# Optimization experiments

Hardware: AMD Instinct MI355X
Metric: run time of the kernel (lower is better)

## Reference

```python
import jax, jax.numpy as jnp
import numpy as np

N_NODES = 50000
N_EDGES = 800000
F_IN = 128   # in_feats
H = 256      # h_feats
C = 32       # num_classes
E_IN = 2     # raw edge feature dim
EPS = 1e-12  # F.normalize eps


def _lin_params(key, fan_in, fan_out):
    kw, kb = jax.random.split(key)
    bound = 1.0 / np.sqrt(fan_in)
    W = jax.random.uniform(kw, (fan_in, fan_out), jnp.float32, -bound, bound)
    b = jax.random.uniform(kb, (fan_out,), jnp.float32, -bound, bound)
    return W, b


def setup_inputs() -> dict:
    key = jax.random.key(0)
    ks = jax.random.split(key, 12)
    inp = {
        "node_feat": jax.random.normal(ks[0], (N_NODES, F_IN), jnp.float32),
        "edge_feat": jax.random.normal(ks[1], (N_EDGES, E_IN), jnp.float32),
        "src": jax.random.randint(ks[2], (N_EDGES,), 0, N_NODES, jnp.int32),
        "dst": jax.random.randint(ks[3], (N_EDGES,), 0, N_NODES, jnp.int32),
    }
    # conv1: SAGEConv(F_IN, H, 2, F_IN)
    inp["We1"], inp["be1"] = _lin_params(ks[4], E_IN, F_IN)        # e_linear
    inp["Wr1a"], inp["br1a"] = _lin_params(ks[5], F_IN, F_IN)      # reduce_linear1
    inp["Wr1b"], inp["br1b"] = _lin_params(ks[6], F_IN, F_IN)      # reduce_linear2
    inp["Wl1"], inp["bl1"] = _lin_params(ks[7], 2 * F_IN, H)       # linear1
    # conv2: SAGEConv(H, C, F_IN, H)
    inp["We2"], inp["be2"] = _lin_params(ks[8], F_IN, H)
    inp["Wr2a"], inp["br2a"] = _lin_params(ks[9], H, H)
    inp["Wr2b"], inp["br2b"] = _lin_params(ks[10], H, H)
    inp["Wl2"], inp["bl2"] = _lin_params(ks[11], 2 * H, C)
    return inp


def _sage_conv(h, e, src, dst, We, be, Wra, bra, Wrb, brb, Wl, bl):
    # edge weight transform
    w = e @ We + be                                    # [E, e_out]
    hs = h[src]                                        # [E, F] gather
    hd = h[dst]
    # per-edge cosine similarity (scalar per edge)
    sn = hs / jnp.maximum(jnp.linalg.norm(hs, axis=1, keepdims=True), EPS)
    dn = hd / jnp.maximum(jnp.linalg.norm(hd, axis=1, keepdims=True), EPS)
    cos = jnp.sum(sn * dn, axis=1, keepdims=True)      # [E, 1]
    m = cos * w * hs                                   # message [E, F]
    # mailbox MLP applied per-edge, then mean-reduce per dst node
    r = jax.nn.relu(m @ Wra + bra)
    r = jax.nn.relu(r @ Wrb + brb)
    s = jax.ops.segment_sum(r, dst, num_segments=N_NODES)
    cnt = jax.ops.segment_sum(jnp.ones((dst.shape[0], 1), r.dtype), dst,
                              num_segments=N_NODES)
    h_N = s / jnp.maximum(cnt, 1.0)                    # zero-degree nodes -> 0
    h_out = jnp.concatenate([h, h_N], axis=1) @ Wl + bl
    return h_out, w


def reference(node_feat, edge_feat, src, dst,
              We1, be1, Wr1a, br1a, Wr1b, br1b, Wl1, bl1,
              We2, be2, Wr2a, br2a, Wr2b, br2b, Wl2, bl2):
    h, e_h = _sage_conv(node_feat, edge_feat, src, dst,
                        We1, be1, Wr1a, br1a, Wr1b, br1b, Wl1, bl1)
    h, e_h = jax.nn.relu(h), jax.nn.relu(e_h)
    h, _ = _sage_conv(h, e_h, src, dst,
                      We2, be2, Wr2a, br2a, Wr2b, br2b, Wl2, bl2)
    return h  # [N_NODES, C] logits
```

## Files before the change

kernel.cpp:

```cpp
#include <hip/hip_runtime.h>
#include <math.h>

#define NN 50000
#define NE 800000

typedef short bf8 __attribute__((ext_vector_type(8)));
typedef short bf4v __attribute__((ext_vector_type(4)));
typedef short bf2v __attribute__((ext_vector_type(2)));
typedef float f4 __attribute__((ext_vector_type(4)));

__device__ __forceinline__ short f2b(float f) {
  unsigned int u = __float_as_uint(f);
  unsigned int r = (u + 0x7FFFu + ((u >> 16) & 1u)) >> 16;
  return (short)(unsigned short)r;
}
__device__ __forceinline__ float b2f(short s) {
  return __uint_as_float(((unsigned int)(unsigned short)s) << 16);
}
__device__ __forceinline__ f4 b2f4(bf4v p) {
  f4 v;
  v[0] = b2f(p[0]); v[1] = b2f(p[1]); v[2] = b2f(p[2]); v[3] = b2f(p[3]);
  return v;
}


__global__ __launch_bounds__(256) void prep_k(
    const float* __restrict__ Wr1a, const float* __restrict__ Wr1b,
    const float* __restrict__ We2,  const float* __restrict__ Wr2a,
    const float* __restrict__ Wr2b, const float* __restrict__ Wl1,
    short* __restrict__ WaT1, short* __restrict__ WbT1,
    short* __restrict__ We2T, short* __restrict__ WaT2,
    short* __restrict__ WbT2, short* __restrict__ Wl1T,
    const float* __restrict__ nf, short* __restrict__ nfb,
    const int* __restrict__ dst, int* __restrict__ cnt)
{
  const int b = blockIdx.x;
  if (b < 1024) {
    const float* in; short* out; int K, N, bb;
    if (b < 64)       { in = Wr1a; out = WaT1; K = 128; N = 128; bb = b; }
    else if (b < 128) { in = Wr1b; out = WbT1; K = 128; N = 128; bb = b - 64; }
    else if (b < 256) { in = We2;  out = We2T; K = 128; N = 256; bb = b - 128; }
    else if (b < 512) { in = Wr2a; out = WaT2; K = 256; N = 256; bb = b - 256; }
    else if (b < 768) { in = Wr2b; out = WbT2; K = 256; N = 256; bb = b - 512; }
    else              { in = Wl1;  out = Wl1T; K = 256; N = 256; bb = b - 768; }
    const int i = bb * 256 + threadIdx.x;
    if (i < K * N) {
      const int n = i / K, k = i - n * K;
      out[i] = f2b(in[(size_t)k * N + n]);
    }
  } else if (b < 7274) {
    const int i = (b - 1024) * 256 + threadIdx.x;
    f4 v = *(const f4*)&nf[(size_t)i * 4];
    bf4v p;
    p[0] = f2b(v[0]); p[1] = f2b(v[1]); p[2] = f2b(v[2]); p[3] = f2b(v[3]);
    *(bf4v*)&nfb[(size_t)i * 4] = p;
  } else {
    const int e = (b - 7274) * 256 + threadIdx.x;
    atomicAdd(&cnt[dst[e]], 1);
  }
}

__global__ __launch_bounds__(256) void norm1_k(const short* __restrict__ nfb,
                                               float* __restrict__ invn) {
  const int node = blockIdx.x * 4 + (threadIdx.x >> 6);
  if (node >= NN) return;
  const int lane = threadIdx.x & 63;
  bf2v hb = *(const bf2v*)&nfb[(size_t)node * 128 + lane * 2];
  float h0 = b2f(hb[0]), h1v = b2f(hb[1]);
  float ss = fmaf(h0, h0, h1v * h1v);
#pragma unroll
  for (int o = 32; o >= 1; o >>= 1) ss += __shfl_xor(ss, o);
  if (lane == 0) invn[node] = 1.f / fmaxf(sqrtf(ss), 1e-12f);
}

__global__ __launch_bounds__(256) void norm2_k(const short* __restrict__ h1b,
                                               float* __restrict__ invn) {
  const int node = blockIdx.x * 4 + (threadIdx.x >> 6);
  if (node >= NN) return;
  const int lane = threadIdx.x & 63;
  f4 h = b2f4(*(const bf4v*)&h1b[(size_t)node * 256 + lane * 4]);
  float ss = 0.f;
#pragma unroll
  for (int r = 0; r < 4; ++r) ss = fmaf(h[r], h[r], ss);
#pragma unroll
  for (int o = 32; o >= 1; o >>= 1) ss += __shfl_xor(ss, o);
  if (lane == 0) invn[node] = 1.f / fmaxf(sqrtf(ss), 1e-12f);
}


__global__ __launch_bounds__(1024) void scanA_k(const int* __restrict__ cnt,
                                                int* __restrict__ off2,
                                                int* __restrict__ bsum) {
  __shared__ int buf[1024];
  const int t = threadIdx.x;
  const int i = blockIdx.x * 1024 + t;
  const int v = (i < NN) ? cnt[i] : 0;
  buf[t] = v;
  __syncthreads();
#pragma unroll
  for (int o = 1; o < 1024; o <<= 1) {
    int x = (t >= o) ? buf[t - o] : 0;
    __syncthreads();
    buf[t] += x;
    __syncthreads();
  }
  if (i < NN) off2[i] = buf[t] - v;
  if (t == 1023) bsum[blockIdx.x] = buf[t];
}

__global__ __launch_bounds__(64) void scanB_k(int* __restrict__ bsum, int nb) {
  const int t = threadIdx.x;
  int v = (t < nb) ? bsum[t] : 0;
#pragma unroll
  for (int o = 1; o < 64; o <<= 1) {
    int x = __shfl_up(v, o);
    if (t >= o) v += x;
  }
  if (t < nb) bsum[t] = v;
}

__global__ __launch_bounds__(256) void scanC_k(int* __restrict__ off2,
                                               const int* __restrict__ bsum) {
  const int i = blockIdx.x * 256 + threadIdx.x;
  if (i >= NN) return;
  const int b = i >> 10;
  if (b) off2[i] += bsum[b - 1];
}

__global__ __launch_bounds__(256) void perm_k(const int* __restrict__ dst,
                                              int* __restrict__ off2,
                                              int* __restrict__ perm,
                                              int* __restrict__ dsts) {
  int e = blockIdx.x * 256 + threadIdx.x;
  if (e >= NE) return;
  int d = dst[e];
  int p = atomicAdd(&off2[d], 1);
  perm[p] = e;
  dsts[p] = d;
}


__global__ __launch_bounds__(512, 8) void edge_mlp1(
    const short* __restrict__ nfb, const float* __restrict__ ef,
    const int* __restrict__ src, const int* __restrict__ perm,
    const int* __restrict__ dsts, const float* __restrict__ invn1,
    const float* __restrict__ We1, const float* __restrict__ be1,
    const short* __restrict__ WaT, const float* __restrict__ ba,
    const short* __restrict__ WbT, const float* __restrict__ bbv,
    float* __restrict__ s1)
{
  __shared__ __align__(16) short Ms[64 * 136];
  __shared__ int dse[64];
  __shared__ int sse[64];
  __shared__ float2 efs[64];
  const int t = threadIdx.x;
  const int e0 = blockIdx.x * 64;
  const int lane = t & 63, wv = t >> 6;

  if (t < 64) {
    const int pe = perm[e0 + t];
    dse[t] = dsts[e0 + t];
    sse[t] = src[pe];
    efs[t] = *(const float2*)&ef[2 * pe];
  }
  __syncthreads();

  {
    const int k2 = lane * 2;
    const float wA0 = We1[k2],       wA1 = We1[k2 + 1];
    const float wB0 = We1[128 + k2], wB1 = We1[128 + k2 + 1];
    const float bE0 = be1[k2],       bE1 = be1[k2 + 1];
    bf2v hbv[8], dbv[8];
#pragma unroll
    for (int i = 0; i < 8; ++i) {
      const int e = wv * 8 + i;
      hbv[i] = *(const bf2v*)&nfb[(size_t)sse[e] * 128 + k2];
      dbv[i] = *(const bf2v*)&nfb[(size_t)dse[e] * 128 + k2];
    }
#pragma unroll
    for (int i = 0; i < 8; ++i) {
      const int e = wv * 8 + i;
      const int s = sse[e];
      const int d = dse[e];
      const float h0 = b2f(hbv[i][0]), h1v = b2f(hbv[i][1]);
      const float g0 = b2f(dbv[i][0]), g1 = b2f(dbv[i][1]);
      float sd = fmaf(h0, g0, h1v * g1);
#pragma unroll
      for (int o = 32; o >= 1; o >>= 1) sd += __shfl_xor(sd, o);
      const float c = sd * invn1[s] * invn1[d];
      const float2 f01 = efs[e];
      const float w0 = fmaf(f01.x, wA0, fmaf(f01.y, wB0, bE0));
      const float w1 = fmaf(f01.x, wA1, fmaf(f01.y, wB1, bE1));
      bf2v pk;
      pk[0] = f2b(c * w0 * h0);
      pk[1] = f2b(c * w1 * h1v);
      *(bf2v*)&Ms[e * 136 + k2] = pk;
    }
  }
  __syncthreads();

  const int lr = lane & 15;
  const int lq = lane >> 4;
  const int n0 = wv * 16;

  f4 acc[4];
#pragma unroll
  for (int b = 0; b < 4; ++b) acc[b] = (f4)0.f;

#pragma unroll
  for (int kc = 0; kc < 128; kc += 32) {
    bf8 aF, bF[4];
    aF = *(const bf8*)&WaT[(size_t)(n0 + lr) * 128 + kc + lq * 8];
#pragma unroll
    for (int b = 0; b < 4; ++b)
      bF[b] = *(const bf8*)&Ms[(b * 16 + lr) * 136 + kc + lq * 8];
#pragma unroll
    for (int b = 0; b < 4; ++b)
      acc[b] = __builtin_amdgcn_mfma_f32_16x16x32_bf16(aF, bF[b], acc[b], 0, 0, 0);
  }
  __syncthreads();

  {
    const int n = n0 + lq * 4;
    f4 bb = *(const f4*)&ba[n];
#pragma unroll
    for (int b = 0; b < 4; ++b) {
      bf4v pk;
#pragma unroll
      for (int r = 0; r < 4; ++r) pk[r] = f2b(fmaxf(acc[b][r] + bb[r], 0.f));
      *(bf4v*)&Ms[(b * 16 + lr) * 136 + n] = pk;
    }
  }
  __syncthreads();

#pragma unroll
  for (int b = 0; b < 4; ++b) acc[b] = (f4)0.f;
#pragma unroll
  for (int kc = 0; kc < 128; kc += 32) {
    bf8 aF, bF[4];
    aF = *(const bf8*)&WbT[(size_t)(n0 + lr) * 128 + kc + lq * 8];
#pragma unroll
    for (int b = 0; b < 4; ++b)
      bF[b] = *(const bf8*)&Ms[(b * 16 + lr) * 136 + kc + lq * 8];
#pragma unroll
    for (int b = 0; b < 4; ++b)
      acc[b] = __builtin_amdgcn_mfma_f32_16x16x32_bf16(aF, bF[b], acc[b], 0, 0, 0);
  }
  __syncthreads();

  {
    const int n = n0 + lq * 4;
    f4 bb = *(const f4*)&bbv[n];
#pragma unroll
    for (int b = 0; b < 4; ++b) {
      bf4v pk;
#pragma unroll
      for (int r = 0; r < 4; ++r) pk[r] = f2b(fmaxf(acc[b][r] + bb[r], 0.f));
      *(bf4v*)&Ms[(b * 16 + lr) * 136 + n] = pk;
    }
  }
  __syncthreads();

  {
    const int f = t & 127;
    const int eb = (t >> 7) * 16;
    float vals[16];
#pragma unroll
    for (int j = 0; j < 16; ++j) vals[j] = b2f(Ms[(eb + j) * 136 + f]);
    float run = 0.f;
    int pd = dse[eb];
#pragma unroll
    for (int j = 0; j < 16; ++j) {
      const int d = dse[eb + j];
      if (d != pd) {
        atomicAdd(&s1[(size_t)pd * 128 + f], run);
        run = 0.f;
        pd = d;
      }
      run += vals[j];
    }
    atomicAdd(&s1[(size_t)pd * 128 + f], run);
  }
}


__global__ __launch_bounds__(512, 6) void edge_mlp2(
    const short* __restrict__ h1b, const float* __restrict__ ef,
    const int* __restrict__ src, const int* __restrict__ perm,
    const int* __restrict__ dsts, const float* __restrict__ invn2,
    const float* __restrict__ We1, const float* __restrict__ be1,
    const short* __restrict__ We2T, const float* __restrict__ be2,
    const short* __restrict__ WaT, const float* __restrict__ ba,
    const short* __restrict__ WbT, const float* __restrict__ bbv,
    float* __restrict__ s2)
{
  __shared__ __align__(16) short U[64 * 264];
  __shared__ int dse[64];
  __shared__ int pes[64];
  __shared__ int sse[64];
  short* Ws  = U;
  short* M2s = U;
  const int t = threadIdx.x;
  const int e0 = blockIdx.x * 64;
  const int lane = t & 63, wv = t >> 6;
  const int lr = lane & 15;
  const int lq = lane >> 4;
  const int n0 = wv * 32;

  if (t < 64) {
    const int pe = perm[e0 + t];
    pes[t] = pe;
    dse[t] = dsts[e0 + t];
    sse[t] = src[pe];
  }
  __syncthreads();

  {
    const int e = t >> 3;
    const int kb = (t & 7) * 16;
    const int pe = pes[e];
    const float f0 = ef[2 * pe], f1 = ef[2 * pe + 1];
#pragma unroll
    for (int j = 0; j < 2; ++j) {
      const int k = kb + j * 8;
      f4 wa0 = *(const f4*)&We1[k];
      f4 wa1 = *(const f4*)&We1[k + 4];
      f4 wb0 = *(const f4*)&We1[128 + k];
      f4 wb1 = *(const f4*)&We1[128 + k + 4];
      f4 b0 = *(const f4*)&be1[k];
      f4 b1 = *(const f4*)&be1[k + 4];
      bf8 pk;
#pragma unroll
      for (int x = 0; x < 4; ++x) {
        pk[x]     = f2b(fmaxf(fmaf(f0, wa0[x], fmaf(f1, wb0[x], b0[x])), 0.f));
        pk[x + 4] = f2b(fmaxf(fmaf(f0, wa1[x], fmaf(f1, wb1[x], b1[x])), 0.f));
      }
      *(bf8*)&Ws[e * 136 + k] = pk;
    }
  }
  __syncthreads();

  f4 acc[2][4];
#pragma unroll
  for (int a = 0; a < 2; ++a)
#pragma unroll
    for (int b = 0; b < 4; ++b) acc[a][b] = (f4)0.f;

#pragma unroll
  for (int kc = 0; kc < 128; kc += 32) {
    bf8 aF[2], bF[4];
#pragma unroll
    for (int a = 0; a < 2; ++a)
      aF[a] = *(const bf8*)&We2T[(size_t)(n0 + a * 16 + lr) * 128 + kc + lq * 8];
#pragma unroll
    for (int b = 0; b < 4; ++b)
      bF[b] = *(const bf8*)&Ws[(b * 16 + lr) * 136 + kc + lq * 8];
#pragma unroll
    for (int a = 0; a < 2; ++a)
#pragma unroll
      for (int b = 0; b < 4; ++b)
        acc[a][b] = __builtin_amdgcn_mfma_f32_16x16x32_bf16(aF[a], bF[b], acc[a][b], 0, 0, 0);
  }
  __syncthreads();

#pragma unroll
  for (int b = 0; b < 4; ++b) {
#pragma unroll
    for (int a = 0; a < 2; ++a) {
      const int n = n0 + a * 16 + lq * 4;
      f4 bb = *(const f4*)&be2[n];
      bf4v pk;
#pragma unroll
      for (int r = 0; r < 4; ++r) pk[r] = f2b(acc[a][b][r] + bb[r]);
      *(bf4v*)&M2s[(b * 16 + lr) * 264 + n] = pk;
    }
  }
  __syncthreads();

  {
    const int k4 = lane * 4;
    bf4v hsv[8], hdv[8];
#pragma unroll
    for (int i = 0; i < 8; ++i) {
      const int e = wv * 8 + i;
      hsv[i] = *(const bf4v*)&h1b[(size_t)sse[e] * 256 + k4];
      hdv[i] = *(const bf4v*)&h1b[(size_t)dse[e] * 256 + k4];
    }
#pragma unroll
    for (int i = 0; i < 8; ++i) {
      const int e = wv * 8 + i;
      const int s = sse[e];
      const int d = dse[e];
      f4 hs = b2f4(hsv[i]);
      f4 hd = b2f4(hdv[i]);
      float sd = 0.f;
#pragma unroll
      for (int r = 0; r < 4; ++r) sd = fmaf(hs[r], hd[r], sd);
#pragma unroll
      for (int o = 32; o >= 1; o >>= 1) sd += __shfl_xor(sd, o);
      const float c = sd * invn2[s] * invn2[d];
      f4 w = b2f4(*(const bf4v*)&M2s[e * 264 + k4]);
      bf4v pk;
#pragma unroll
      for (int r = 0; r < 4; ++r) pk[r] = f2b(w[r] * c * hs[r]);
      *(bf4v*)&M2s[e * 264 + k4] = pk;
    }
  }
  __syncthreads();

#pragma unroll
  for (int a = 0; a < 2; ++a)
#pragma unroll
    for (int b = 0; b < 4; ++b) acc[a][b] = (f4)0.f;
  for (int kc = 0; kc < 256; kc += 32) {
    bf8 aF[2], bF[4];
#pragma unroll
    for (int a = 0; a < 2; ++a)
      aF[a] = *(const bf8*)&WaT[(size_t)(n0 + a * 16 + lr) * 256 + kc + lq * 8];
#pragma unroll
    for (int b = 0; b < 4; ++b)
      bF[b] = *(const bf8*)&M2s[(b * 16 + lr) * 264 + kc + lq * 8];
#pragma unroll
    for (int a = 0; a < 2; ++a)
#pragma unroll
      for (int b = 0; b < 4; ++b)
        acc[a][b] = __builtin_amdgcn_mfma_f32_16x16x32_bf16(aF[a], bF[b], acc[a][b], 0, 0, 0);
  }
  __syncthreads();

#pragma unroll
  for (int a = 0; a < 2; ++a) {
    const int n = n0 + a * 16 + lq * 4;
    f4 bb = *(const f4*)&ba[n];
#pragma unroll
    for (int b = 0; b < 4; ++b) {
      bf4v pk;
#pragma unroll
      for (int r = 0; r < 4; ++r) pk[r] = f2b(fmaxf(acc[a][b][r] + bb[r], 0.f));
      *(bf4v*)&M2s[(b * 16 + lr) * 264 + n] = pk;
    }
  }
  __syncthreads();

#pragma unroll
  for (int a = 0; a < 2; ++a)
#pragma unroll
    for (int b = 0; b < 4; ++b) acc[a][b] = (f4)0.f;
  for (int kc = 0; kc < 256; kc += 32) {
    bf8 aF[2], bF[4];
#pragma unroll
    for (int a = 0; a < 2; ++a)
      aF[a] = *(const bf8*)&WbT[(size_t)(n0 + a * 16 + lr) * 256 + kc + lq * 8];
#pragma unroll
    for (int b = 0; b < 4; ++b)
      bF[b] = *(const bf8*)&M2s[(b * 16 + lr) * 264 + kc + lq * 8];
#pragma unroll
    for (int a = 0; a < 2; ++a)
#pragma unroll
      for (int b = 0; b < 4; ++b)
        acc[a][b] = __builtin_amdgcn_mfma_f32_16x16x32_bf16(aF[a], bF[b], acc[a][b], 0, 0, 0);
  }
  __syncthreads();

  float* RF = (float*)M2s;
#pragma unroll
  for (int h = 0; h < 2; ++h) {
    if ((wv >> 2) == h) {
#pragma unroll
      for (int a = 0; a < 2; ++a) {
        const int n = n0 + a * 16 + lq * 4;
        f4 bb = *(const f4*)&bbv[n];
#pragma unroll
        for (int b = 0; b < 4; ++b) {
          f4 v;
#pragma unroll
          for (int r = 0; r < 4; ++r) v[r] = fmaxf(acc[a][b][r] + bb[r], 0.f);
          *(f4*)&RF[(b * 16 + lr) * 132 + (n - h * 128)] = v;
        }
      }
    }
    __syncthreads();
    {
      const int f = t & 127;
      const int eb = (t >> 7) * 16;
      float run = 0.f;
      int pd = dse[eb];
#pragma unroll 4
      for (int e = eb; e < eb + 16; ++e) {
        const int d = dse[e];
        if (d != pd) {
          atomicAdd(&s2[(size_t)pd * 256 + h * 128 + f], run);
          run = 0.f;
          pd = d;
        }
        run += RF[e * 132 + f];
      }
      atomicAdd(&s2[(size_t)pd * 256 + h * 128 + f], run);
    }
    __syncthreads();
  }
}


__global__ __launch_bounds__(256, 3) void h1m_k(
    const float* __restrict__ nf, const float* __restrict__ s1,
    const int* __restrict__ cnt, const short* __restrict__ Wl1T,
    const float* __restrict__ bl1, short* __restrict__ h1b)
{
  __shared__ __align__(16) short As[64 * 264];
  const int t = threadIdx.x;
  const int v0 = blockIdx.x * 64;

  {
    const int row = t >> 2;
    const int kb = (t & 3) * 64;
    int gn = v0 + row;
    if (gn >= NN) gn = NN - 1;
    const float inv = 1.f / fmaxf((float)cnt[gn], 1.f);
#pragma unroll
    for (int j = 0; j < 64; j += 8) {
      const int k = kb + j;
      f4 x0, x1;
      if (k < 128) {
        x0 = *(const f4*)&nf[(size_t)gn * 128 + k];
        x1 = *(const f4*)&nf[(size_t)gn * 128 + k + 4];
      } else {
        x0 = *(const f4*)&s1[(size_t)gn * 128 + (k - 128)];
        x1 = *(const f4*)&s1[(size_t)gn * 128 + (k - 124)];
#pragma unroll
        for (int x = 0; x < 4; ++x) { x0[x] *= inv; x1[x] *= inv; }
      }
      bf8 pk;
#pragma unroll
      for (int x = 0; x < 4; ++x) { pk[x] = f2b(x0[x]); pk[x + 4] = f2b(x1[x]); }
      *(bf8*)&As[row * 264 + k] = pk;
    }
  }
  __syncthreads();

  const int lane = t & 63, wv = t >> 6;
  const int lr = lane & 15;
  const int lq = lane >> 4;
  const int n0 = wv * 64;

  f4 acc[4][4];
#pragma unroll
  for (int a = 0; a < 4; ++a)
#pragma unroll
    for (int b = 0; b < 4; ++b) acc[a][b] = (f4)0.f;

  for (int kc = 0; kc < 256; kc += 32) {
    bf8 aF[4], bF[4];
#pragma unroll
    for (int a = 0; a < 4; ++a)
      aF[a] = *(const bf8*)&Wl1T[(size_t)(n0 + a * 16 + lr) * 256 + kc + lq * 8];
#pragma unroll
    for (int b = 0; b < 4; ++b)
      bF[b] = *(const bf8*)&As[(b * 16 + lr) * 264 + kc + lq * 8];
#pragma unroll
    for (int a = 0; a < 4; ++a)
#pragma unroll
      for (int b = 0; b < 4; ++b)
        acc[a][b] = __builtin_amdgcn_mfma_f32_16x16x32_bf16(aF[a], bF[b], acc[a][b], 0, 0, 0);
  }

#pragma unroll
  for (int b = 0; b < 4; ++b) {
    const int gn = v0 + b * 16 + lr;
    if (gn >= NN) continue;
#pragma unroll
    for (int a = 0; a < 4; ++a) {
      const int n = n0 + a * 16 + lq * 4;
      f4 bb = *(const f4*)&bl1[n];
      bf4v pk;
      pk[0] = f2b(fmaxf(acc[a][b][0] + bb[0], 0.f));
      pk[1] = f2b(fmaxf(acc[a][b][1] + bb[1], 0.f));
      pk[2] = f2b(fmaxf(acc[a][b][2] + bb[2], 0.f));
      pk[3] = f2b(fmaxf(acc[a][b][3] + bb[3], 0.f));
      *(bf4v*)&h1b[(size_t)gn * 256 + n] = pk;
    }
  }
}


__global__ __launch_bounds__(256) void out_k(
    const short* __restrict__ h1b, const float* __restrict__ s2,
    const int* __restrict__ cnt, const float* __restrict__ Wl2,
    const float* __restrict__ bl2, float* __restrict__ out)
{
  __shared__ float A8[8][512];
  const int n0 = blockIdx.x * 8;
  const int tx = threadIdx.x;
  const int ty = threadIdx.y;
  const int t = ty * 32 + tx;
  const int row = t >> 5;
  const int k0 = (t & 31) * 16;
  const int n = n0 + row;
  const float inv = 1.0f / fmaxf((float)cnt[n], 1.0f);
#pragma unroll
  for (int i = 0; i < 16; i += 4) {
    int k = k0 + i;
    f4 v;
    if (k < 256) {
      v = b2f4(*(const bf4v*)&h1b[(size_t)n * 256 + k]);
    } else {
      v = *(const f4*)&s2[(size_t)n * 256 + (k - 256)];
      v[0] *= inv; v[1] *= inv; v[2] *= inv; v[3] *= inv;
    }
    *(f4*)&A8[row][k] = v;
  }
  __syncthreads();
  float acc = bl2[tx];
#pragma unroll 8
  for (int k = 0; k < 512; k++) acc = fmaf(A8[ty][k], Wl2[(size_t)k * 32 + tx], acc);
  out[(size_t)(n0 + ty) * 32 + tx] = acc;
}


extern "C" void kernel_launch(void* const* d_in, const int* in_sizes, int n_in,
                              void* d_out, int out_size, void* d_ws, size_t ws_size,
                              hipStream_t stream) {
  const float* nf   = (const float*)d_in[0];
  const float* ef   = (const float*)d_in[1];
  const int*   src  = (const int*)d_in[2];
  const int*   dst  = (const int*)d_in[3];
  const float* We1  = (const float*)d_in[4];
  const float* be1  = (const float*)d_in[5];
  const float* Wr1a = (const float*)d_in[6];
  const float* br1a = (const float*)d_in[7];
  const float* Wr1b = (const float*)d_in[8];
  const float* br1b = (const float*)d_in[9];
  const float* Wl1  = (const float*)d_in[10];
  const float* bl1  = (const float*)d_in[11];
  const float* We2  = (const float*)d_in[12];
  const float* be2  = (const float*)d_in[13];
  const float* Wr2a = (const float*)d_in[14];
  const float* br2a = (const float*)d_in[15];
  const float* Wr2b = (const float*)d_in[16];
  const float* br2b = (const float*)d_in[17];
  const float* Wl2  = (const float*)d_in[18];
  const float* bl2  = (const float*)d_in[19];

  float* ws = (float*)d_ws;
  float* s1   = ws;
  float* s2   = s1 + (size_t)NN * 128;
  int*   cnt  = (int*)(s2 + (size_t)NN * 256);
  short* h1b  = (short*)(cnt + NN);
  short* nfb  = h1b + (size_t)NN * 256;
  short* WaT1 = nfb + (size_t)NN * 128;
  short* WbT1 = WaT1 + 128 * 128;
  short* We2T = WbT1 + 128 * 128;
  short* WaT2 = We2T + 256 * 128;
  short* WbT2 = WaT2 + 256 * 256;
  short* Wl1T = WbT2 + 256 * 256;
  int*   off2 = (int*)(Wl1T + 256 * 256);
  int*   perm = off2 + NN;
  int*   dsts = perm + NE;
  float* invn1 = (float*)(dsts + NE);
  float* invn2 = invn1 + NN;
  int*   bsum  = (int*)(invn2 + NN);

  size_t need = ((size_t)NN * 128 + (size_t)NN * 256 + NN) * 4 +
                ((size_t)NN * 256 + (size_t)NN * 128 +
                 (size_t)128 * 128 * 2 + (size_t)256 * 128 +
                 (size_t)256 * 256 * 3) * 2 +
                ((size_t)NN + 2 * (size_t)NE + 2 * (size_t)NN) * 4 + 64 * 4;
  if (ws_size < need) return;

  hipMemsetAsync(s1, 0, ((size_t)NN * 128 + (size_t)NN * 256 + NN) * 4, stream);

  prep_k<<<10399, 256, 0, stream>>>(Wr1a, Wr1b, We2, Wr2a, Wr2b, Wl1,
                                    WaT1, WbT1, We2T, WaT2, WbT2, Wl1T,
                                    nf, nfb, dst, cnt);
  norm1_k<<<(NN + 3) / 4, 256, 0, stream>>>(nfb, invn1);

  const int nb = (NN + 1023) / 1024;
  scanA_k<<<nb, 1024, 0, stream>>>(cnt, off2, bsum);
  scanB_k<<<1, 64, 0, stream>>>(bsum, nb);
  scanC_k<<<(NN + 255) / 256, 256, 0, stream>>>(off2, bsum);
  perm_k<<<NE / 256, 256, 0, stream>>>(dst, off2, perm, dsts);

  edge_mlp1<<<NE / 64, 512, 0, stream>>>(nfb, ef, src, perm, dsts, invn1,
                                         We1, be1, WaT1, br1a, WbT1, br1b, s1);

  h1m_k<<<(NN + 63) / 64, 256, 0, stream>>>(nf, s1, cnt, Wl1T, bl1, h1b);
  norm2_k<<<(NN + 3) / 4, 256, 0, stream>>>(h1b, invn2);

  edge_mlp2<<<NE / 64, 512, 0, stream>>>(h1b, ef, src, perm, dsts, invn2,
                                         We1, be1, We2T, be2, WaT2, br2a,
                                         WbT2, br2b, s2);

  out_k<<<NN / 8, dim3(32, 8), 0, stream>>>(h1b, s2, cnt, Wl2, bl2, (float*)d_out);
}
```

Measured before the change: 1.184 ms.

## Fuse edge-weight epilogue with cosine scaling and overlap gathers with edge MLP

```diff
diff --git a/kernel.cpp b/kernel.cpp
--- a/kernel.cpp
+++ b/kernel.cpp
@@ -1,4 +1,5 @@
 #include <hip/hip_runtime.h>
+#include <hip/hip_bf16.h>
 #include <math.h>
 
 #define NN 50000
@@ -10,9 +11,9 @@
 typedef float f4 __attribute__((ext_vector_type(4)));
 
 __device__ __forceinline__ short f2b(float f) {
-  unsigned int u = __float_as_uint(f);
-  unsigned int r = (u + 0x7FFFu + ((u >> 16) & 1u)) >> 16;
-  return (short)(unsigned short)r;
+  union { __hip_bfloat16 h; short s; } u;
+  u.h = __float2bfloat16(f);
+  return u.s;
 }
 __device__ __forceinline__ float b2f(short s) {
   return __uint_as_float(((unsigned int)(unsigned short)s) << 16);
@@ -298,6 +299,7 @@
   __shared__ int dse[64];
   __shared__ int pes[64];
   __shared__ int sse[64];
+  __shared__ float csh[64];
   short* Ws  = U;
   short* M2s = U;
   const int t = threadIdx.x;
@@ -315,79 +317,43 @@
   }
   __syncthreads();
 
-  {
-    const int e = t >> 3;
-    const int kb = (t & 7) * 16;
-    const int pe = pes[e];
-    const float f0 = ef[2 * pe], f1 = ef[2 * pe + 1];
-#pragma unroll
-    for (int j = 0; j < 2; ++j) {
-      const int k = kb + j * 8;
-      f4 wa0 = *(const f4*)&We1[k];
-      f4 wa1 = *(const f4*)&We1[k + 4];
-      f4 wb0 = *(const f4*)&We1[128 + k];
-      f4 wb1 = *(const f4*)&We1[128 + k + 4];
-      f4 b0 = *(const f4*)&be1[k];
-      f4 b1 = *(const f4*)&be1[k + 4];
-      bf8 pk;
-#pragma unroll
-      for (int x = 0; x < 4; ++x) {
-        pk[x]     = f2b(fmaxf(fmaf(f0, wa0[x], fmaf(f1, wb0[x], b0[x])), 0.f));
-        pk[x + 4] = f2b(fmaxf(fmaf(f0, wa1[x], fmaf(f1, wb1[x], b1[x])), 0.f));
-      }
-      *(bf8*)&Ws[e * 136 + k] = pk;
-    }
-  }
-  __syncthreads();
-
-  f4 acc[2][4];
-#pragma unroll
-  for (int a = 0; a < 2; ++a)
-#pragma unroll
-    for (int b = 0; b < 4; ++b) acc[a][b] = (f4)0.f;
-
-#pragma unroll
-  for (int kc = 0; kc < 128; kc += 32) {
-    bf8 aF[2], bF[4];
-#pragma unroll
-    for (int a = 0; a < 2; ++a)
-      aF[a] = *(const bf8*)&We2T[(size_t)(n0 + a * 16 + lr) * 128 + kc + lq * 8];
-#pragma unroll
-    for (int b = 0; b < 4; ++b)
-      bF[b] = *(const bf8*)&Ws[(b * 16 + lr) * 136 + kc + lq * 8];
-#pragma unroll
-    for (int a = 0; a < 2; ++a)
-#pragma unroll
-      for (int b = 0; b < 4; ++b)
-        acc[a][b] = __builtin_amdgcn_mfma_f32_16x16x32_bf16(aF[a], bF[b], acc[a][b], 0, 0, 0);
-  }
-  __syncthreads();
-
-#pragma unroll
-  for (int b = 0; b < 4; ++b) {
-#pragma unroll
-    for (int a = 0; a < 2; ++a) {
-      const int n = n0 + a * 16 + lq * 4;
-      f4 bb = *(const f4*)&be2[n];
-      bf4v pk;
-#pragma unroll
-      for (int r = 0; r < 4; ++r) pk[r] = f2b(acc[a][b][r] + bb[r]);
-      *(bf4v*)&M2s[(b * 16 + lr) * 264 + n] = pk;
-    }
-  }
-  __syncthreads();
-
+  float creg = 0.f;
   {
     const int k4 = lane * 4;
-    bf4v hsv[8], hdv[8];
-#pragma unroll
-    for (int i = 0; i < 8; ++i) {
+    bf4v hsv[4], hdv[4];
+#pragma unroll
+    for (int i = 0; i < 4; ++i) {
       const int e = wv * 8 + i;
       hsv[i] = *(const bf4v*)&h1b[(size_t)sse[e] * 256 + k4];
       hdv[i] = *(const bf4v*)&h1b[(size_t)dse[e] * 256 + k4];
     }
-#pragma unroll
-    for (int i = 0; i < 8; ++i) {
+
+    {
+      const int e = t >> 3;
+      const int kb = (t & 7) * 16;
+      const int pe = pes[e];
+      const float f0 = ef[2 * pe], f1 = ef[2 * pe + 1];
+#pragma unroll
+      for (int j = 0; j < 2; ++j) {
+        const int k = kb + j * 8;
+        f4 wa0 = *(const f4*)&We1[k];
+        f4 wa1 = *(const f4*)&We1[k + 4];
+        f4 wb0 = *(const f4*)&We1[128 + k];
+        f4 wb1 = *(const f4*)&We1[128 + k + 4];
+        f4 b0 = *(const f4*)&be1[k];
+        f4 b1 = *(const f4*)&be1[k + 4];
+        bf8 pk;
+#pragma unroll
+        for (int x = 0; x < 4; ++x) {
+          pk[x]     = f2b(fmaxf(fmaf(f0, wa0[x], fmaf(f1, wb0[x], b0[x])), 0.f));
+          pk[x + 4] = f2b(fmaxf(fmaf(f0, wa1[x], fmaf(f1, wb1[x], b1[x])), 0.f));
+        }
+        *(bf8*)&Ws[e * 136 + k] = pk;
+      }
+    }
+
+#pragma unroll
+    for (int i = 0; i < 4; ++i) {
       const int e = wv * 8 + i;
       const int s = sse[e];
       const int d = dse[e];
@@ -399,11 +365,86 @@
 #pragma unroll
       for (int o = 32; o >= 1; o >>= 1) sd += __shfl_xor(sd, o);
       const float c = sd * invn2[s] * invn2[d];
-      f4 w = b2f4(*(const bf4v*)&M2s[e * 264 + k4]);
-      bf4v pk;
-#pragma unroll
-      for (int r = 0; r < 4; ++r) pk[r] = f2b(w[r] * c * hs[r]);
-      *(bf4v*)&M2s[e * 264 + k4] = pk;
+      if (lane == i) creg = c;
+    }
+#pragma unroll
+    for (int i = 0; i < 4; ++i) {
+      const int e = wv * 8 + 4 + i;
+      hsv[i] = *(const bf4v*)&h1b[(size_t)sse[e] * 256 + k4];
+      hdv[i] = *(const bf4v*)&h1b[(size_t)dse[e] * 256 + k4];
+    }
+#pragma unroll
+    for (int i = 0; i < 4; ++i) {
+      const int e = wv * 8 + 4 + i;
+      const int s = sse[e];
+      const int d = dse[e];
+      f4 hs = b2f4(hsv[i]);
+      f4 hd = b2f4(hdv[i]);
+      float sd = 0.f;
+#pragma unroll
+      for (int r = 0; r < 4; ++r) sd = fmaf(hs[r], hd[r], sd);
+#pragma unroll
+      for (int o = 32; o >= 1; o >>= 1) sd += __shfl_xor(sd, o);
+      const float c = sd * invn2[s] * invn2[d];
+      if (lane == 4 + i) creg = c;
+    }
+  }
+  if (lane < 8) csh[wv * 8 + lane] = creg;
+  __syncthreads();
+
+  f4 acc[2][4];
+#pragma unroll
+  for (int a = 0; a < 2; ++a)
+#pragma unroll
+    for (int b = 0; b < 4; ++b) acc[a][b] = (f4)0.f;
+
+#pragma unroll
+  for (int kc = 0; kc < 128; kc += 32) {
+    bf8 aF[2], bF[4];
+#pragma unroll
+    for (int a = 0; a < 2; ++a)
+      aF[a] = *(const bf8*)&We2T[(size_t)(n0 + a * 16 + lr) * 128 + kc + lq * 8];
+#pragma unroll
+    for (int b = 0; b < 4; ++b)
+      bF[b] = *(const bf8*)&Ws[(b * 16 + lr) * 136 + kc + lq * 8];
+#pragma unroll
+    for (int a = 0; a < 2; ++a)
+#pragma unroll
+      for (int b = 0; b < 4; ++b)
+        acc[a][b] = __builtin_amdgcn_mfma_f32_16x16x32_bf16(aF[a], bF[b], acc[a][b], 0, 0, 0);
+  }
+  __syncthreads();
+
+  {
+    f4 bb0 = *(const f4*)&be2[n0 + lq * 4];
+    f4 bb1 = *(const f4*)&be2[n0 + 16 + lq * 4];
+#pragma unroll
+    for (int bq = 0; bq < 2; ++bq) {
+      bf4v hsv[4];
+#pragma unroll
+      for (int b2 = 0; b2 < 2; ++b2)
+#pragma unroll
+        for (int a = 0; a < 2; ++a) {
+          const int b = bq * 2 + b2;
+          hsv[b2 * 2 + a] = *(const bf4v*)&h1b[(size_t)sse[b * 16 + lr] * 256 +
+                                               n0 + a * 16 + lq * 4];
+        }
+#pragma unroll
+      for (int b2 = 0; b2 < 2; ++b2) {
+        const int b = bq * 2 + b2;
+        const float c = csh[b * 16 + lr];
+#pragma unroll
+        for (int a = 0; a < 2; ++a) {
+          const int n = n0 + a * 16 + lq * 4;
+          f4 bb = (a == 0) ? bb0 : bb1;
+          f4 hs = b2f4(hsv[b2 * 2 + a]);
+          bf4v pk;
+#pragma unroll
+          for (int r = 0; r < 4; ++r)
+            pk[r] = f2b((acc[a][b][r] + bb[r]) * c * hs[r]);
+          *(bf4v*)&M2s[(b * 16 + lr) * 264 + n] = pk;
+        }
+      }
     }
   }
   __syncthreads();
```

Result: slower. 1.253 ms (+5.8%).
